# Kernel optimization log

Measured on AMD Instinct MI355X. Metric: run time of the kernel, lower is better.

The kernel has to match this reference:

```python
import jax, jax.numpy as jnp
import numpy as np

KX = jnp.array([[-1., 0., 1.], [-2., 0., 2.], [-1., 0., 1.]], dtype=jnp.float32).reshape(1, 1, 3, 3)
KY = jnp.array([[1., 2., 1.], [0., 0., 0.], [-1., -2., -1.]], dtype=jnp.float32).reshape(1, 1, 3, 3)

def _sobel(x, k):
    # x: [B,1,H,W], k: [1,1,3,3]; stride 1, padding 1 -> same spatial size
    return jax.lax.conv_general_dilated(
        x, k, window_strides=(1, 1), padding=((1, 1), (1, 1)),
        dimension_numbers=('NCHW', 'OIHW', 'NCHW'))

def setup_inputs() -> dict:
    key = jax.random.key(0)
    k1, k2 = jax.random.split(key)
    B, C, H, W = 32, 1, 512, 512
    output = jax.random.normal(k1, (B, C, H, W), dtype=jnp.float32)
    target = jax.random.normal(k2, (B, C, H, W), dtype=jnp.float32)
    return {"output": output, "target": target}

def reference(output, target):
    gx_t = _sobel(target, KX)
    gy_t = _sobel(target, KY)
    gx_o = _sobel(output, KX)
    gy_o = _sobel(output, KY)
    grad_loss = jnp.mean((gx_t - gx_o) ** 2) + jnp.mean((gy_t - gy_o) ** 2)
    return grad_loss
```

## Files before the change

### kernel.cpp

```cpp
#include <hip/hip_runtime.h>


#define BATCH 32
#define HH 512
#define WW 512
#define RW 16
#define TPB 256
#define NPART (BATCH * (HH / RW))

__global__ __launch_bounds__(TPB) void sobel_partial_kernel(
    const float* __restrict__ out_img,
    const float* __restrict__ tgt_img,
    float* __restrict__ partials)
{
    const int tid  = threadIdx.x;
    const int lane = tid & 63;
    const int w    = blockIdx.x * (TPB / 64) + (tid >> 6);
    const int img  = w >> 5;
    const int y0   = (w & 31) * RW;

    const size_t base = (size_t)img * HH * WW;
    const float* ob = out_img + base;
    const float* tb = tgt_img + base;
    const int x1 = lane * 4;
    const int x2 = 256 + lane * 4;

    float hs[3][8];
    float hd[3][8];
    float acc = 0.f;

    #pragma unroll
    for (int i = 0; i < RW + 2; ++i) {
        const int g   = y0 - 1 + i;
        const int cur = i % 3;

        float4 d1, d2;
        if ((unsigned)g < (unsigned)HH) {
            const float* orow = ob + (size_t)g * WW;
            const float* trow = tb + (size_t)g * WW;
            const float4 o1 = *(const float4*)(orow + x1);
            const float4 t1 = *(const float4*)(trow + x1);
            const float4 o2 = *(const float4*)(orow + x2);
            const float4 t2 = *(const float4*)(trow + x2);
            d1 = make_float4(t1.x - o1.x, t1.y - o1.y, t1.z - o1.z, t1.w - o1.w);
            d2 = make_float4(t2.x - o2.x, t2.y - o2.y, t2.z - o2.z, t2.w - o2.w);
        } else {
            d1 = make_float4(0.f, 0.f, 0.f, 0.f);
            d2 = make_float4(0.f, 0.f, 0.f, 0.f);
        }

        float dl1 = __shfl_up(d1.w, 1, 64);
        if (lane == 0) dl1 = 0.f;
        const float s2x = __shfl(d2.x, 0, 64);
        float dr1 = __shfl_down(d1.x, 1, 64);
        if (lane == 63) dr1 = s2x;
        const float s1w = __shfl(d1.w, 63, 64);
        float dl2 = __shfl_up(d2.w, 1, 64);
        if (lane == 0) dl2 = s1w;
        float dr2 = __shfl_down(d2.x, 1, 64);
        if (lane == 63) dr2 = 0.f;

        hs[cur][0] = fmaf(2.f, d1.x, dl1 + d1.y);  hd[cur][0] = d1.y - dl1;
        hs[cur][1] = fmaf(2.f, d1.y, d1.x + d1.z); hd[cur][1] = d1.z - d1.x;
        hs[cur][2] = fmaf(2.f, d1.z, d1.y + d1.w); hd[cur][2] = d1.w - d1.y;
        hs[cur][3] = fmaf(2.f, d1.w, d1.z + dr1);  hd[cur][3] = dr1 - d1.z;
        hs[cur][4] = fmaf(2.f, d2.x, dl2 + d2.y);  hd[cur][4] = d2.y - dl2;
        hs[cur][5] = fmaf(2.f, d2.y, d2.x + d2.z); hd[cur][5] = d2.z - d2.x;
        hs[cur][6] = fmaf(2.f, d2.z, d2.y + d2.w); hd[cur][6] = d2.w - d2.y;
        hs[cur][7] = fmaf(2.f, d2.w, d2.z + dr2);  hd[cur][7] = dr2 - d2.z;

        if (i >= 2) {
            const int top = (i - 2) % 3;
            const int mid = (i - 1) % 3;
            #pragma unroll
            for (int j = 0; j < 8; ++j) {
                const float gx = fmaf(2.f, hd[mid][j], hd[top][j] + hd[cur][j]);
                const float gy = hs[top][j] - hs[cur][j];
                acc = fmaf(gx, gx, acc);
                acc = fmaf(gy, gy, acc);
            }
        }
    }

    #pragma unroll
    for (int off = 32; off > 0; off >>= 1)
        acc += __shfl_down(acc, off, 64);
    if (lane == 0)
        partials[w] = acc;
}

__global__ __launch_bounds__(TPB) void reduce_partials_kernel(
    const float* __restrict__ partials, float* __restrict__ out)
{
    const int tid = threadIdx.x;
    float s = 0.f;
    #pragma unroll
    for (int i = 0; i < NPART / TPB; ++i)
        s += partials[tid + i * TPB];
    #pragma unroll
    for (int off = 32; off > 0; off >>= 1)
        s += __shfl_down(s, off, 64);
    __shared__ float wsum[TPB / 64];
    if ((tid & 63) == 0) wsum[tid >> 6] = s;
    __syncthreads();
    if (tid == 0)
        out[0] = (wsum[0] + wsum[1] + wsum[2] + wsum[3])
               * (1.0f / ((float)BATCH * HH * WW));
}

extern "C" void kernel_launch(void* const* d_in, const int* in_sizes, int n_in,
                              void* d_out, int out_size, void* d_ws, size_t ws_size,
                              hipStream_t stream) {
    (void)in_sizes; (void)n_in; (void)ws_size; (void)out_size;
    const float* out_img = (const float*)d_in[0];
    const float* tgt_img = (const float*)d_in[1];
    float* partials = (float*)d_ws;
    float* res = (float*)d_out;

    sobel_partial_kernel<<<NPART / (TPB / 64), TPB, 0, stream>>>(out_img, tgt_img, partials);
    reduce_partials_kernel<<<1, TPB, 0, stream>>>(partials, res);
}
```

Before: 19.84 us.

## Split sobel work into half-width 8-row strips with all loads hoisted upfront

```diff
diff --git a/kernel.cpp b/kernel.cpp
--- a/kernel.cpp
+++ b/kernel.cpp
@@ -4,76 +4,74 @@
 #define BATCH 32
 #define HH 512
 #define WW 512
-#define RW 16
+#define RW 8
 #define TPB 256
-#define NPART (BATCH * (HH / RW))
+#define WPI 128
+#define NPART (BATCH * WPI)
+#define NBLK (NPART / 4)
 
-__global__ __launch_bounds__(TPB) void sobel_partial_kernel(
+__global__ __launch_bounds__(TPB, 4) void sobel_partial_kernel(
     const float* __restrict__ out_img,
     const float* __restrict__ tgt_img,
     float* __restrict__ partials)
 {
     const int tid  = threadIdx.x;
     const int lane = tid & 63;
-    const int w    = blockIdx.x * (TPB / 64) + (tid >> 6);
-    const int img  = w >> 5;
-    const int y0   = (w & 31) * RW;
+    const int b    = (blockIdx.x & 7) * (NBLK / 8) + (blockIdx.x >> 3);
+    const int w    = b * (TPB / 64) + (tid >> 6);
+    const int img  = w >> 7;
+    const int r    = w & (WPI - 1);
+    const int y0   = (r >> 1) * RW;
+    const int xh   = r & 1;
+    const int x0   = (xh << 8) + lane * 4;
 
     const size_t base = (size_t)img * HH * WW;
     const float* ob = out_img + base;
     const float* tb = tgt_img + base;
-    const int x1 = lane * 4;
-    const int x2 = 256 + lane * 4;
 
-    float hs[3][8];
-    float hd[3][8];
-    float acc = 0.f;
+    const int  seamcol = xh ? 255 : 256;
+    const bool loader  = xh ? (lane == 0) : (lane == 63);
 
+    float4 dv[RW + 2];
+    float  sm[RW + 2];
     #pragma unroll
     for (int i = 0; i < RW + 2; ++i) {
-        const int g   = y0 - 1 + i;
+        const int g = y0 - 1 + i;
+        if ((unsigned)g < (unsigned)HH) {
+            const size_t ro = (size_t)g * WW;
+            const float4 o = *(const float4*)(ob + ro + x0);
+            const float4 t = *(const float4*)(tb + ro + x0);
+            dv[i] = make_float4(t.x - o.x, t.y - o.y, t.z - o.z, t.w - o.w);
+            float s = 0.f;
+            if (loader) s = tb[ro + seamcol] - ob[ro + seamcol];
+            sm[i] = s;
+        } else {
+            dv[i] = make_float4(0.f, 0.f, 0.f, 0.f);
+            sm[i] = 0.f;
+        }
+    }
+
+    float hs[3][4], hd[3][4];
+    float acc = 0.f;
+    #pragma unroll
+    for (int i = 0; i < RW + 2; ++i) {
+        const float4 d = dv[i];
+        float dl = __shfl_up(d.w, 1, 64);
+        if (lane == 0)  dl = sm[i];
+        float dr = __shfl_down(d.x, 1, 64);
+        if (lane == 63) dr = sm[i];
+
         const int cur = i % 3;
-
-        float4 d1, d2;
-        if ((unsigned)g < (unsigned)HH) {
-            const float* orow = ob + (size_t)g * WW;
-            const float* trow = tb + (size_t)g * WW;
-            const float4 o1 = *(const float4*)(orow + x1);
-            const float4 t1 = *(const float4*)(trow + x1);
-            const float4 o2 = *(const float4*)(orow + x2);
-            const float4 t2 = *(const float4*)(trow + x2);
-            d1 = make_float4(t1.x - o1.x, t1.y - o1.y, t1.z - o1.z, t1.w - o1.w);
-            d2 = make_float4(t2.x - o2.x, t2.y - o2.y, t2.z - o2.z, t2.w - o2.w);
-        } else {
-            d1 = make_float4(0.f, 0.f, 0.f, 0.f);
-            d2 = make_float4(0.f, 0.f, 0.f, 0.f);
-        }
-
-        float dl1 = __shfl_up(d1.w, 1, 64);
-        if (lane == 0) dl1 = 0.f;
-        const float s2x = __shfl(d2.x, 0, 64);
-        float dr1 = __shfl_down(d1.x, 1, 64);
-        if (lane == 63) dr1 = s2x;
-        const float s1w = __shfl(d1.w, 63, 64);
-        float dl2 = __shfl_up(d2.w, 1, 64);
-        if (lane == 0) dl2 = s1w;
-        float dr2 = __shfl_down(d2.x, 1, 64);
-        if (lane == 63) dr2 = 0.f;
-
-        hs[cur][0] = fmaf(2.f, d1.x, dl1 + d1.y);  hd[cur][0] = d1.y - dl1;
-        hs[cur][1] = fmaf(2.f, d1.y, d1.x + d1.z); hd[cur][1] = d1.z - d1.x;
-        hs[cur][2] = fmaf(2.f, d1.z, d1.y + d1.w); hd[cur][2] = d1.w - d1.y;
-        hs[cur][3] = fmaf(2.f, d1.w, d1.z + dr1);  hd[cur][3] = dr1 - d1.z;
-        hs[cur][4] = fmaf(2.f, d2.x, dl2 + d2.y);  hd[cur][4] = d2.y - dl2;
-        hs[cur][5] = fmaf(2.f, d2.y, d2.x + d2.z); hd[cur][5] = d2.z - d2.x;
-        hs[cur][6] = fmaf(2.f, d2.z, d2.y + d2.w); hd[cur][6] = d2.w - d2.y;
-        hs[cur][7] = fmaf(2.f, d2.w, d2.z + dr2);  hd[cur][7] = dr2 - d2.z;
+        hs[cur][0] = fmaf(2.f, d.x, dl  + d.y);  hd[cur][0] = d.y - dl;
+        hs[cur][1] = fmaf(2.f, d.y, d.x + d.z);  hd[cur][1] = d.z - d.x;
+        hs[cur][2] = fmaf(2.f, d.z, d.y + d.w);  hd[cur][2] = d.w - d.y;
+        hs[cur][3] = fmaf(2.f, d.w, d.z + dr);   hd[cur][3] = dr  - d.z;
 
         if (i >= 2) {
             const int top = (i - 2) % 3;
             const int mid = (i - 1) % 3;
             #pragma unroll
-            for (int j = 0; j < 8; ++j) {
+            for (int j = 0; j < 4; ++j) {
                 const float gx = fmaf(2.f, hd[mid][j], hd[top][j] + hd[cur][j]);
                 const float gy = hs[top][j] - hs[cur][j];
                 acc = fmaf(gx, gx, acc);
@@ -95,8 +93,10 @@
     const int tid = threadIdx.x;
     float s = 0.f;
     #pragma unroll
-    for (int i = 0; i < NPART / TPB; ++i)
-        s += partials[tid + i * TPB];
+    for (int i = 0; i < NPART / (TPB * 4); ++i) {
+        const float4 v = *(const float4*)(partials + (tid + i * TPB) * 4);
+        s += (v.x + v.y) + (v.z + v.w);
+    }
     #pragma unroll
     for (int off = 32; off > 0; off >>= 1)
         s += __shfl_down(s, off, 64);
@@ -117,6 +117,6 @@
     float* partials = (float*)d_ws;
     float* res = (float*)d_out;
 
-    sobel_partial_kernel<<<NPART / (TPB / 64), TPB, 0, stream>>>(out_img, tgt_img, partials);
+    sobel_partial_kernel<<<NBLK, TPB, 0, stream>>>(out_img, tgt_img, partials);
     reduce_partials_kernel<<<1, TPB, 0, stream>>>(partials, res);
 }
```

Result: slower. 20.47 us (+3.2%).
